# Kernel optimization log

Hardware: AMD Instinct MI355X
Metric: run time of the kernel (lower is better)

Reference implementation:

```python
import jax, jax.numpy as jnp
import numpy as np

L, N, M = 128, 512, 256   # batch-like dim, recurrence length, feature dim (M_size1)
TK, H = 4, 8              # num_blocks, num_heads
DH = M // H
EPS = 1e-5


def setup_inputs() -> dict:
    key = jax.random.key(0)
    ks = jax.random.split(key, 8)
    s = 0.05  # scale raw-randn params for numerical stability
    return {
        "x": jax.random.normal(ks[0], (L, N, M), jnp.float32),
        "weight": jax.random.normal(ks[1], (M, M), jnp.float32) * s,
        "Wqkv": jax.random.normal(ks[2], (TK, 3, H, DH, M), jnp.float32) * s,
        "Wo": jax.random.normal(ks[3], (TK, M, M), jnp.float32) * s,
        "ln_g": jnp.ones((M,), jnp.float32),
        "ln_b": jnp.zeros((M,), jnp.float32),
        "lnz_g": jnp.ones((M,), jnp.float32),
        "lnz_b": jnp.zeros((M,), jnp.float32),
        "fc1_w": jax.random.normal(ks[4], (4 * M, M), jnp.float32) / np.float32(np.sqrt(M)),
        "fc1_b": jnp.zeros((4 * M,), jnp.float32),
        "fc2_w": jax.random.normal(ks[5], (M, 4 * M), jnp.float32) / np.float32(np.sqrt(4 * M)),
        "fc2_b": jnp.zeros((M,), jnp.float32),
    }


def _ln(x, g, b):
    mu = x.mean(-1, keepdims=True)
    var = x.var(-1, keepdims=True)  # biased variance, as torch LayerNorm
    return (x - mu) * jax.lax.rsqrt(var + EPS) * g + b


def _pos_bias(dtype):
    # bias[j, z]   = sin(j / 10000**(2z/M)) for even z
    # bias[j, z+1] = cos(j / 10000**(2z/M))
    pos = jnp.arange(N, dtype=dtype)                      # j
    z = jnp.arange(0, M, 2, dtype=dtype)                  # even indices
    ang = pos[:, None] / (10000.0 ** (2.0 * z / M))       # (N, M/2)
    return jnp.stack([jnp.sin(ang), jnp.cos(ang)], axis=-1).reshape(N, M)


def reference(x, weight, Wqkv, Wo, ln_g, ln_b, lnz_g, lnz_b, fc1_w, fc1_b, fc2_w, fc2_b):
    # savespace: (L, N, M); positional bias depends only on (j, feature)
    s = jnp.einsum('lm,ijm->ijl', weight, x) + _pos_bias(x.dtype)[None]
    inv_sqrt_dh = np.float32(1.0 / np.sqrt(DH))
    for a in range(TK):
        qkv = jnp.einsum('xhdm,ijm->xijhd', Wqkv[a], _ln(s, ln_g, ln_b))
        q, k, v = qkv[0], qkv[1], qkv[2]                  # each (L, N, H, DH)
        rsa = jnp.einsum('ijhd,ijhd->ijh', q * inv_sqrt_dh, k)
        imv = rsa[..., None] * v                           # (L, N, H, DH)
        imv = jnp.cumsum(imv, axis=1)                      # retention recurrence over j
        s = jnp.einsum('nm,ijm->ijn', Wo[a], imv.reshape(L, N, M)) + s
        s = _ln(s, lnz_g, lnz_b) + s
        h = jax.nn.gelu(s @ fc1_w.T + fc1_b, approximate=False)
        s = h @ fc2_w.T + fc2_b
    return s
```

## Files before the change

### kernel.cpp

```cpp
#include <hip/hip_runtime.h>

typedef unsigned int u32;
typedef unsigned short u16;
typedef _Float16 f16;
typedef __attribute__((ext_vector_type(8))) _Float16 f16x8;
typedef __attribute__((ext_vector_type(4))) float f32x4;
typedef __attribute__((ext_vector_type(4))) u16 u16x4;

#define L_ 128
#define N_ 512
#define M_ 256
#define TK_ 4
#define H_ 8
#define R_ (L_*N_)
#define FF_ 1024

__device__ __forceinline__ u16 f2h(float v){ f16 h=(f16)v; return __builtin_bit_cast(u16,h); }
__device__ __forceinline__ float h2f(u16 b){ return (float)__builtin_bit_cast(f16,b); }
__device__ __forceinline__ f32x4 mfmah(f16x8 a, f16x8 b, f32x4 c){
  return __builtin_amdgcn_mfma_f32_16x16x32_f16(a,b,c,0,0,0);
}
__device__ __forceinline__ float gelu_f(float x){
  float u = x*(0.7978845608f + 0.0356774081f*x*x);
  float e = __expf(u + u);
  float r = __builtin_amdgcn_rcpf(e + 1.f);
  return x - x*r;
}


__global__ void k_bias(float* __restrict__ bias){
  int j = blockIdx.x, l = threadIdx.x;
  int t = l>>1;
  float base = expf(-0.14391156831212757f * (float)t);
  float ang = (float)j * base;
  bias[j*M_ + l] = (l&1) ? cosf(ang) : sinf(ang);
}

__global__ void k_pack(const float* __restrict__ src, u16* __restrict__ dst, int K){
  int b = blockIdx.x; int nk = K>>6; int cg = b/nk, k64 = b%nk;
  int t = threadIdx.x;
  int st = t>>6, g = (t>>4)&3, lr = t&15;
  const float* sp = src + (cg*16+lr)*K + k64*64 + st*32 + g*8;
  f16x8 hv;
  #pragma unroll
  for (int e=0;e<8;e++) hv[e] = (f16)sp[e];
  *(f16x8*)(dst + b*1024 + t*8) = hv;
}

__global__ void k_pack_qkv(const float* __restrict__ w, u16* __restrict__ dst){
  int b = blockIdx.x;
  int a = b/192; int rmn = b%192; int grp = rmn>>2, k64 = rmn&3;
  int hd = grp/6, cidx = grp%6;
  int t = threadIdx.x;
  int st = t>>6, g = (t>>4)&3, lr = t&15;
  int cl = cidx*16 + lr;
  int x = cl>>5, d = cl&31;
  const float* sp = w + (((a*3+x)*H_+hd)*32 + d)*M_ + k64*64 + st*32 + g*8;
  f16x8 hv;
  #pragma unroll
  for (int e=0;e<8;e++) hv[e] = (f16)sp[e];
  *(f16x8*)(dst + b*1024 + t*8) = hv;
}

__device__ __forceinline__ void stageA16(const u16* __restrict__ src, u16* __restrict__ Abuf,
                                         int rowbase, int tid){
  int row = tid>>3, skh = tid&7;
  int k64 = skh>>1, st = skh&1;
  int rg = row>>4, lr = row&15;
  const u16* sp = src + (rowbase+row)*M_ + k64*64 + st*32;
  u16* dp = Abuf + (k64*4+rg)*1024 + st*512 + lr*8;
  #pragma unroll
  for (int gg=0;gg<4;gg++)
    *(uint4*)(dp + gg*128) = *(const uint4*)(sp + gg*8);
}

__global__ __launch_bounds__(512) void k_init(const float* __restrict__ X, const u16* __restrict__ Wf,
    const float* __restrict__ bias, const float* __restrict__ lg, const float* __restrict__ lb,
    float* __restrict__ out, u16* __restrict__ P1){
  __shared__ __align__(16) u16 Abuf[16*1024];
  __shared__ float zs[8][64][2];
  int tid = threadIdx.x;
  int wx = tid>>6, lane = tid&63;
  int g = lane>>4, lr = lane&15;
  int lo = g*128 + lr*8;
  int rowbase = blockIdx.x*64;
  {
    int row = tid>>3, skh = tid&7;
    int k64 = skh>>1, st = skh&1;
    int rg = row>>4, slr = row&15;
    const float* sp = X + (rowbase+row)*M_ + k64*64 + st*32;
    u16* dp = Abuf + (k64*4+rg)*1024 + st*512 + slr*8;
    #pragma unroll
    for (int gg=0;gg<4;gg++){
      f16x8 hv;
      #pragma unroll
      for (int e=0;e<8;e++) hv[e] = (f16)sp[gg*8+e];
      *(f16x8*)(dp + gg*128) = hv;
    }
  }
  __syncthreads();
  f32x4 acc[4][2];
  #pragma unroll
  for (int i=0;i<4;i++){ acc[i][0]=0.f; acc[i][1]=0.f; }
  #pragma unroll
  for (int k64=0;k64<4;k64++)
    #pragma unroll
    for (int st=0;st<2;st++){
      f16x8 a[4], b[2];
      #pragma unroll
      for (int i=0;i<4;i++) a[i] = *(const f16x8*)(Abuf + (k64*4 + i)*1024 + st*512 + lo);
      #pragma unroll
      for (int j=0;j<2;j++) b[j] = *(const f16x8*)(Wf + ((wx*2+j)*4 + k64)*1024 + st*512 + lo);
      #pragma unroll
      for (int i=0;i<4;i++)
        #pragma unroll
        for (int j=0;j<2;j++) acc[i][j] = mfmah(a[i], b[j], acc[i][j]);
    }
  #pragma unroll
  for (int i=0;i<4;i++)
    #pragma unroll
    for (int j=0;j<2;j++)
      #pragma unroll
      for (int r=0;r<4;r++){
        int row = rowbase + i*16 + g*4 + r;
        int col = wx*32 + j*16 + lr;
        acc[i][j][r] += bias[(row & (N_-1))*M_ + col];
        out[row*M_ + col] = acc[i][j][r];
      }
  #pragma unroll
  for (int i=0;i<4;i++)
    #pragma unroll
    for (int r=0;r<4;r++){
      float ps = 0.f, qs = 0.f;
      #pragma unroll
      for (int j=0;j<2;j++){ float t = acc[i][j][r]; ps += t; qs += t*t; }
      ps += __shfl_xor(ps,1); qs += __shfl_xor(qs,1);
      ps += __shfl_xor(ps,2); qs += __shfl_xor(qs,2);
      ps += __shfl_xor(ps,4); qs += __shfl_xor(qs,4);
      ps += __shfl_xor(ps,8); qs += __shfl_xor(qs,8);
      if (lr == 0){
        int rowl = i*16 + g*4 + r;
        zs[wx][rowl][0] = ps;
        zs[wx][rowl][1] = qs;
      }
    }
  __syncthreads();
  #pragma unroll
  for (int i=0;i<4;i++)
    #pragma unroll
    for (int r=0;r<4;r++){
      int rowl = i*16 + g*4 + r;
      float sum=0.f, sq=0.f;
      #pragma unroll
      for (int q=0;q<8;q++){ sum += zs[q][rowl][0]; sq += zs[q][rowl][1]; }
      float mean = sum*(1.f/M_);
      float var  = sq*(1.f/M_) - mean*mean;
      float rstd = rsqrtf(var + 1e-5f);
      int row = rowbase + rowl;
      #pragma unroll
      for (int j=0;j<2;j++){
        int col = wx*32 + j*16 + lr;
        P1[row*M_ + col] = f2h((acc[i][j][r]-mean)*rstd*lg[col] + lb[col]);
      }
    }
}

__global__ __launch_bounds__(512) void k_qkv(const u16* __restrict__ P1, const u16* __restrict__ Wq,
    u16* __restrict__ imv){
  __shared__ __align__(16) u16 Abuf[16*1024];
  int tid = threadIdx.x;
  int hd = tid>>6, lane = tid&63;
  int g = lane>>4, lr = lane&15;
  int lo = g*128 + lr*8;
  int rowbase = blockIdx.x*64;
  stageA16(P1, Abuf, rowbase, tid);
  __syncthreads();
  f32x4 acc[4][6];
  #pragma unroll
  for (int i=0;i<4;i++)
    #pragma unroll
    for (int c=0;c<6;c++) acc[i][c] = 0.f;
  const u16* Wb = Wq + hd*6*4096;
  #pragma unroll
  for (int k64=0;k64<4;k64++)
    #pragma unroll
    for (int st=0;st<2;st++){
      f16x8 a[4];
      #pragma unroll
      for (int i=0;i<4;i++) a[i] = *(const f16x8*)(Abuf + (k64*4 + i)*1024 + st*512 + lo);
      #pragma unroll
      for (int c=0;c<6;c++){
        f16x8 b = *(const f16x8*)(Wb + (c*4 + k64)*1024 + st*512 + lo);
        #pragma unroll
        for (int i=0;i<4;i++) acc[i][c] = mfmah(a[i], b, acc[i][c]);
      }
    }
  const float isd = 0.17677669529663687f;
  #pragma unroll
  for (int i=0;i<4;i++){
    f32x4 p = acc[i][0]*acc[i][2] + acc[i][1]*acc[i][3];
    #pragma unroll
    for (int r=0;r<4;r++){
      float v = p[r];
      v += __shfl_xor(v,1); v += __shfl_xor(v,2);
      v += __shfl_xor(v,4); v += __shfl_xor(v,8);
      float rsa = v * isd;
      int row = rowbase + i*16 + g*4 + r;
      imv[row*M_ + hd*32 + lr]      = f2h(rsa*acc[i][4][r]);
      imv[row*M_ + hd*32 + 16 + lr] = f2h(rsa*acc[i][5][r]);
    }
  }
}

__global__ __launch_bounds__(256) void k_scan(const u16* __restrict__ imv, u16* __restrict__ P1){
  __shared__ float tot[4][64];
  int bi = blockIdx.x;
  int i = bi>>2, mc = bi&3;
  int tid = threadIdx.x;
  int ml = tid&63, jc = tid>>6;
  int m = mc*64 + ml;
  int base = i*N_*M_ + jc*128*M_ + m;
  float acc = 0.f;
  for (int jb=0;jb<128;jb+=8){
    float t[8];
    #pragma unroll
    for (int u=0;u<8;u++) t[u] = h2f(imv[base + (jb+u)*M_]);
    #pragma unroll
    for (int u=0;u<8;u++) acc += t[u];
  }
  tot[jc][ml] = acc;
  __syncthreads();
  float pre = 0.f;
  #pragma unroll
  for (int q=0;q<3;q++) if (q<jc) pre += tot[q][ml];
  acc = pre;
  for (int jb=0;jb<128;jb+=8){
    float t[8];
    #pragma unroll
    for (int u=0;u<8;u++) t[u] = h2f(imv[base + (jb+u)*M_]);
    #pragma unroll
    for (int u=0;u<8;u++){ acc += t[u]; P1[base + (jb+u)*M_] = f2h(acc); }
  }
}

__global__ __launch_bounds__(512) void k_wo(u16* __restrict__ P1, const u16* __restrict__ Wf,
    const float* __restrict__ sold, const float* __restrict__ lg, const float* __restrict__ lb){
  __shared__ __align__(16) u16 Abuf[16*1024];
  __shared__ float zs[8][64][2];
  int tid = threadIdx.x;
  int wx = tid>>6, lane = tid&63;
  int g = lane>>4, lr = lane&15;
  int lo = g*128 + lr*8;
  int rowbase = blockIdx.x*64;
  stageA16(P1, Abuf, rowbase, tid);
  __syncthreads();
  f32x4 acc[4][2];
  #pragma unroll
  for (int i=0;i<4;i++){ acc[i][0]=0.f; acc[i][1]=0.f; }
  #pragma unroll
  for (int k64=0;k64<4;k64++)
    #pragma unroll
    for (int st=0;st<2;st++){
      f16x8 a[4], b[2];
      #pragma unroll
      for (int i=0;i<4;i++) a[i] = *(const f16x8*)(Abuf + (k64*4 + i)*1024 + st*512 + lo);
      #pragma unroll
      for (int j=0;j<2;j++) b[j] = *(const f16x8*)(Wf + ((wx*2+j)*4 + k64)*1024 + st*512 + lo);
      #pragma unroll
      for (int i=0;i<4;i++)
        #pragma unroll
        for (int j=0;j<2;j++) acc[i][j] = mfmah(a[i], b[j], acc[i][j]);
    }
  #pragma unroll
  for (int i=0;i<4;i++)
    #pragma unroll
    for (int j=0;j<2;j++)
      #pragma unroll
      for (int r=0;r<4;r++){
        int row = rowbase + i*16 + g*4 + r;
        int col = wx*32 + j*16 + lr;
        acc[i][j][r] += sold[row*M_ + col];
      }
  #pragma unroll
  for (int i=0;i<4;i++)
    #pragma unroll
    for (int r=0;r<4;r++){
      float ps = 0.f, qs = 0.f;
      #pragma unroll
      for (int j=0;j<2;j++){ float t = acc[i][j][r]; ps += t; qs += t*t; }
      ps += __shfl_xor(ps,1); qs += __shfl_xor(qs,1);
      ps += __shfl_xor(ps,2); qs += __shfl_xor(qs,2);
      ps += __shfl_xor(ps,4); qs += __shfl_xor(qs,4);
      ps += __shfl_xor(ps,8); qs += __shfl_xor(qs,8);
      if (lr == 0){
        int rowl = i*16 + g*4 + r;
        zs[wx][rowl][0] = ps;
        zs[wx][rowl][1] = qs;
      }
    }
  __syncthreads();
  #pragma unroll
  for (int i=0;i<4;i++)
    #pragma unroll
    for (int r=0;r<4;r++){
      int rowl = i*16 + g*4 + r;
      float sum=0.f, sq=0.f;
      #pragma unroll
      for (int q=0;q<8;q++){ sum += zs[q][rowl][0]; sq += zs[q][rowl][1]; }
      float mean = sum*(1.f/M_);
      float var  = sq*(1.f/M_) - mean*mean;
      float rstd = rsqrtf(var + 1e-5f);
      int row = rowbase + rowl;
      #pragma unroll
      for (int j=0;j<2;j++){
        int col = wx*32 + j*16 + lr;
        float zv = acc[i][j][r];
        P1[row*M_ + col] = f2h((zv-mean)*rstd*lg[col] + lb[col] + zv);
      }
    }
}

__global__ __launch_bounds__(512) void k_fc(u16* __restrict__ P1,
    const u16* __restrict__ W1f, const float* __restrict__ b1,
    const u16* __restrict__ W2f, const float* __restrict__ b2,
    const float* __restrict__ lg, const float* __restrict__ lb,
    float* __restrict__ out){
  __shared__ __align__(16) u16 Abuf[16*1024];
  __shared__ __align__(16) u16 Hbuf[64*128];
  __shared__ float zs[4][64][2];
  int tid = threadIdx.x;
  int wid = tid>>6, lane = tid&63;
  int wr = wid>>2, wc = wid&3;
  int g = lane>>4, lr = lane&15;
  int lo = g*128 + lr*8;
  int rowbase = blockIdx.x*64;
  stageA16(P1, Abuf, rowbase, tid);
  __syncthreads();
  f32x4 acc2[2][4];
  #pragma unroll
  for (int i=0;i<2;i++)
    #pragma unroll
    for (int j=0;j<4;j++) acc2[i][j] = 0.f;
  for (int c=0;c<8;c++){
    f32x4 acc1[2][2];
    #pragma unroll
    for (int i=0;i<2;i++){ acc1[i][0]=0.f; acc1[i][1]=0.f; }
    #pragma unroll
    for (int k64=0;k64<4;k64++)
      #pragma unroll
      for (int st=0;st<2;st++){
        f16x8 aw[2], bs[2];
        #pragma unroll
        for (int i=0;i<2;i++) aw[i] = *(const f16x8*)(W1f + ((c*8 + wc*2 + i)*4 + k64)*1024 + st*512 + lo);
        #pragma unroll
        for (int j=0;j<2;j++) bs[j] = *(const f16x8*)(Abuf + (k64*4 + wr*2 + j)*1024 + st*512 + lo);
        #pragma unroll
        for (int i=0;i<2;i++)
          #pragma unroll
          for (int j=0;j<2;j++) acc1[i][j] = mfmah(aw[i], bs[j], acc1[i][j]);
      }
    __syncthreads();
    #pragma unroll
    for (int i=0;i<2;i++){
      int fl = wc*32 + i*16 + g*4;
      int kc = fl>>6, kloc = fl&63;
      float4 b1v = *(const float4*)(b1 + c*128 + fl);
      float bb[4] = {b1v.x, b1v.y, b1v.z, b1v.w};
      #pragma unroll
      for (int j=0;j<2;j++){
        int row = wr*32 + j*16 + lr;
        u16x4 hv;
        #pragma unroll
        for (int r=0;r<4;r++)
          hv[r] = f2h(gelu_f(acc1[i][j][r] + bb[r]));
        int phys = ((kloc>>3) ^ row) & 7;
        *(u16x4*)(Hbuf + row*128 + kc*64 + phys*8 + (kloc&7)) = hv;
      }
    }
    __syncthreads();
    #pragma unroll
    for (int kcl=0;kcl<2;kcl++)
      #pragma unroll
      for (int st=0;st<2;st++){
        f16x8 ah[2], bb2[4];
        #pragma unroll
        for (int j=0;j<4;j++)
          bb2[j] = *(const f16x8*)(W2f + ((wc*4+j)*16 + c*2 + kcl)*1024 + st*512 + lo);
        #pragma unroll
        for (int i=0;i<2;i++){
          int hrow = wr*32 + i*16 + lr;
          int phys = (((st<<2)|g) ^ hrow) & 7;
          ah[i] = *(const f16x8*)(Hbuf + hrow*128 + kcl*64 + phys*8);
        }
        #pragma unroll
        for (int i=0;i<2;i++)
          #pragma unroll
          for (int j=0;j<4;j++) acc2[i][j] = mfmah(ah[i], bb2[j], acc2[i][j]);
      }
  }
  #pragma unroll
  for (int i=0;i<2;i++)
    #pragma unroll
    for (int j=0;j<4;j++)
      #pragma unroll
      for (int r=0;r<4;r++){
        int row = rowbase + wr*32 + i*16 + g*4 + r;
        int col = wc*64 + j*16 + lr;
        acc2[i][j][r] += b2[col];
        out[row*M_ + col] = acc2[i][j][r];
      }
  #pragma unroll
  for (int i=0;i<2;i++)
    #pragma unroll
    for (int r=0;r<4;r++){
      float ps = 0.f, qs = 0.f;
      #pragma unroll
      for (int j=0;j<4;j++){ float t = acc2[i][j][r]; ps += t; qs += t*t; }
      ps += __shfl_xor(ps,1); qs += __shfl_xor(qs,1);
      ps += __shfl_xor(ps,2); qs += __shfl_xor(qs,2);
      ps += __shfl_xor(ps,4); qs += __shfl_xor(qs,4);
      ps += __shfl_xor(ps,8); qs += __shfl_xor(qs,8);
      if (lr == 0){
        int rowl = wr*32 + i*16 + g*4 + r;
        zs[wc][rowl][0] = ps;
        zs[wc][rowl][1] = qs;
      }
    }
  __syncthreads();
  #pragma unroll
  for (int i=0;i<2;i++)
    #pragma unroll
    for (int r=0;r<4;r++){
      int rowl = wr*32 + i*16 + g*4 + r;
      float sum=0.f, sq=0.f;
      #pragma unroll
      for (int q=0;q<4;q++){ sum += zs[q][rowl][0]; sq += zs[q][rowl][1]; }
      float mean = sum*(1.f/M_);
      float var  = sq*(1.f/M_) - mean*mean;
      float rstd = rsqrtf(var + 1e-5f);
      int row = rowbase + rowl;
      #pragma unroll
      for (int j=0;j<4;j++){
        int col = wc*64 + j*16 + lr;
        P1[row*M_ + col] = f2h((acc2[i][j][r]-mean)*rstd*lg[col] + lb[col]);
      }
    }
}

extern "C" void kernel_launch(void* const* d_in, const int* in_sizes, int n_in,
                              void* d_out, int out_size, void* d_ws, size_t ws_size,
                              hipStream_t stream){
  const float* x      = (const float*)d_in[0];
  const float* weight = (const float*)d_in[1];
  const float* wqkv   = (const float*)d_in[2];
  const float* wo     = (const float*)d_in[3];
  const float* ln_g   = (const float*)d_in[4];
  const float* ln_b   = (const float*)d_in[5];
  const float* lnz_g  = (const float*)d_in[6];
  const float* lnz_b  = (const float*)d_in[7];
  const float* fc1_w  = (const float*)d_in[8];
  const float* fc1_b  = (const float*)d_in[9];
  const float* fc2_w  = (const float*)d_in[10];
  const float* fc2_b  = (const float*)d_in[11];
  float* out = (float*)d_out;
  char* ws = (char*)d_ws;
  size_t off = 0;
  u16* wqkvf   = (u16*)(ws + off); off += 1572864;
  u16* wof     = (u16*)(ws + off); off += 524288;
  u16* fc1f    = (u16*)(ws + off); off += 524288;
  u16* fc2f    = (u16*)(ws + off); off += 524288;
  u16* weightf = (u16*)(ws + off); off += 131072;
  float* bias  = (float*)(ws + off); off += 524288;
  u16* P1      = (u16*)(ws + off); off += 33554432;
  u16* imv     = (u16*)(ws + off); off += 33554432;

  k_bias<<<N_, M_, 0, stream>>>(bias);
  k_pack<<<64, 128, 0, stream>>>(weight, weightf, 256);
  k_pack_qkv<<<768, 128, 0, stream>>>(wqkv, wqkvf);
  k_pack<<<256, 128, 0, stream>>>(wo, wof, 256);
  k_pack<<<256, 128, 0, stream>>>(fc1_w, fc1f, 256);
  k_pack<<<256, 128, 0, stream>>>(fc2_w, fc2f, 1024);
  k_init<<<R_/64, 512, 0, stream>>>(x, weightf, bias, ln_g, ln_b, out, P1);
  for (int a=0; a<TK_; a++){
    k_qkv<<<R_/64, 512, 0, stream>>>(P1, wqkvf + a*196608, imv);
    k_scan<<<L_*4, 256, 0, stream>>>(imv, P1);
    k_wo<<<R_/64, 512, 0, stream>>>(P1, wof + a*65536, out, lnz_g, lnz_b);
    k_fc<<<R_/64, 512, 0, stream>>>(P1, fc1f, fc1_b, fc2f, fc2_b, ln_g, ln_b, out);
  }
}
```

Measured before the change: 887.0 us.

## Shrink FC kernel to 32-row tiles and double-buffer the hidden tile

The fused FC1-GELU-FC2 kernel now processes 32 rows per block with 4 waves instead of 64 rows with 8 waves, and stages the input tile with its own inline loop. The hidden-activation buffer is double-buffered across chunks, which lets one of the two barriers per chunk be dropped. The smaller blocks and lower shared memory use should raise occupancy and cut synchronisation stalls. The cost is that each block reuses the FC weights over fewer rows, so weight traffic from L2 roughly doubles.

```diff
diff --git a/kernel.cpp b/kernel.cpp
--- a/kernel.cpp
+++ b/kernel.cpp
@@ -320,21 +320,29 @@
     }
 }
 
-__global__ __launch_bounds__(512) void k_fc(u16* __restrict__ P1,
+__global__ __launch_bounds__(256) void k_fc(u16* __restrict__ P1,
     const u16* __restrict__ W1f, const float* __restrict__ b1,
     const u16* __restrict__ W2f, const float* __restrict__ b2,
     const float* __restrict__ lg, const float* __restrict__ lb,
     float* __restrict__ out){
-  __shared__ __align__(16) u16 Abuf[16*1024];
-  __shared__ __align__(16) u16 Hbuf[64*128];
-  __shared__ float zs[4][64][2];
+  __shared__ __align__(16) u16 Abuf[8*1024];
+  __shared__ __align__(16) u16 Hbuf[2][32*128];
+  __shared__ float zs[4][32][2];
   int tid = threadIdx.x;
-  int wid = tid>>6, lane = tid&63;
-  int wr = wid>>2, wc = wid&3;
+  int wc = tid>>6, lane = tid&63;
   int g = lane>>4, lr = lane&15;
   int lo = g*128 + lr*8;
-  int rowbase = blockIdx.x*64;
-  stageA16(P1, Abuf, rowbase, tid);
+  int rowbase = blockIdx.x*32;
+  {
+    int row = tid>>3, skh = tid&7;
+    int k64 = skh>>1, st = skh&1;
+    int rg = row>>4, slr = row&15;
+    const u16* sp = P1 + (rowbase+row)*M_ + k64*64 + st*32;
+    u16* dp = Abuf + (k64*2+rg)*1024 + st*512 + slr*8;
+    #pragma unroll
+    for (int gg=0;gg<4;gg++)
+      *(uint4*)(dp + gg*128) = *(const uint4*)(sp + gg*8);
+  }
   __syncthreads();
   f32x4 acc2[2][4];
   #pragma unroll
@@ -342,6 +350,7 @@
     #pragma unroll
     for (int j=0;j<4;j++) acc2[i][j] = 0.f;
   for (int c=0;c<8;c++){
+    u16* Hb = Hbuf[c&1];
     f32x4 acc1[2][2];
     #pragma unroll
     for (int i=0;i<2;i++){ acc1[i][0]=0.f; acc1[i][1]=0.f; }
@@ -353,13 +362,12 @@
         #pragma unroll
         for (int i=0;i<2;i++) aw[i] = *(const f16x8*)(W1f + ((c*8 + wc*2 + i)*4 + k64)*1024 + st*512 + lo);
         #pragma unroll
-        for (int j=0;j<2;j++) bs[j] = *(const f16x8*)(Abuf + (k64*4 + wr*2 + j)*1024 + st*512 + lo);
+        for (int j=0;j<2;j++) bs[j] = *(const f16x8*)(Abuf + (k64*2 + j)*1024 + st*512 + lo);
         #pragma unroll
         for (int i=0;i<2;i++)
           #pragma unroll
           for (int j=0;j<2;j++) acc1[i][j] = mfmah(aw[i], bs[j], acc1[i][j]);
       }
-    __syncthreads();
     #pragma unroll
     for (int i=0;i<2;i++){
       int fl = wc*32 + i*16 + g*4;
@@ -368,13 +376,13 @@
       float bb[4] = {b1v.x, b1v.y, b1v.z, b1v.w};
       #pragma unroll
       for (int j=0;j<2;j++){
-        int row = wr*32 + j*16 + lr;
+        int row = j*16 + lr;
         u16x4 hv;
         #pragma unroll
         for (int r=0;r<4;r++)
           hv[r] = f2h(gelu_f(acc1[i][j][r] + bb[r]));
         int phys = ((kloc>>3) ^ row) & 7;
-        *(u16x4*)(Hbuf + row*128 + kc*64 + phys*8 + (kloc&7)) = hv;
+        *(u16x4*)(Hb + row*128 + kc*64 + phys*8 + (kloc&7)) = hv;
       }
     }
     __syncthreads();
@@ -388,9 +396,9 @@
           bb2[j] = *(const f16x8*)(W2f + ((wc*4+j)*16 + c*2 + kcl)*1024 + st*512 + lo);
         #pragma unroll
         for (int i=0;i<2;i++){
-          int hrow = wr*32 + i*16 + lr;
+          int hrow = i*16 + lr;
           int phys = (((st<<2)|g) ^ hrow) & 7;
-          ah[i] = *(const f16x8*)(Hbuf + hrow*128 + kcl*64 + phys*8);
+          ah[i] = *(const f16x8*)(Hb + hrow*128 + kcl*64 + phys*8);
         }
         #pragma unroll
         for (int i=0;i<2;i++)
@@ -404,7 +412,7 @@
     for (int j=0;j<4;j++)
       #pragma unroll
       for (int r=0;r<4;r++){
-        int row = rowbase + wr*32 + i*16 + g*4 + r;
+        int row = rowbase + i*16 + g*4 + r;
         int col = wc*64 + j*16 + lr;
         acc2[i][j][r] += b2[col];
         out[row*M_ + col] = acc2[i][j][r];
@@ -421,7 +429,7 @@
       ps += __shfl_xor(ps,4); qs += __shfl_xor(qs,4);
       ps += __shfl_xor(ps,8); qs += __shfl_xor(qs,8);
       if (lr == 0){
-        int rowl = wr*32 + i*16 + g*4 + r;
+        int rowl = i*16 + g*4 + r;
         zs[wc][rowl][0] = ps;
         zs[wc][rowl][1] = qs;
       }
@@ -431,7 +439,7 @@
   for (int i=0;i<2;i++)
     #pragma unroll
     for (int r=0;r<4;r++){
-      int rowl = wr*32 + i*16 + g*4 + r;
+      int rowl = i*16 + g*4 + r;
       float sum=0.f, sq=0.f;
       #pragma unroll
       for (int q=0;q<4;q++){ sum += zs[q][rowl][0]; sq += zs[q][rowl][1]; }
@@ -485,6 +493,6 @@
     k_qkv<<<R_/64, 512, 0, stream>>>(P1, wqkvf + a*196608, imv);
     k_scan<<<L_*4, 256, 0, stream>>>(imv, P1);
     k_wo<<<R_/64, 512, 0, stream>>>(P1, wof + a*65536, out, lnz_g, lnz_b);
-    k_fc<<<R_/64, 512, 0, stream>>>(P1, fc1f, fc1_b, fc2f, fc2_b, ln_g, ln_b, out);
-  }
-}
+    k_fc<<<R_/32, 256, 0, stream>>>(P1, fc1f, fc1_b, fc2f, fc2_b, ln_g, ln_b, out);
+  }
+}
```

After: 1.014 ms. +14.4%, slower.
